# Optimization experiments

Measured on AMD Instinct MI355X. Metric: run time of the kernel, lower is better.

Reference implementation:

```python
import jax, jax.numpy as jnp
import numpy as np

NUM_HEADS = 8
QKV_DIM = 32
DIM = 256
MULTI_Q = QKV_DIM * NUM_HEADS  # 256
BN_EPS = 1e-5


def conv1x1_bn(x, W, gamma, beta, mean, var):
    # 1x1 conv (no bias) followed by BatchNorm2d in eval mode.
    y = jnp.einsum('bchw,oc->bohw', x, W)
    inv = gamma / jnp.sqrt(var + BN_EPS)
    return y * inv[None, :, None, None] + (beta - mean * inv)[None, :, None, None]


def setup_inputs() -> dict:
    key = jax.random.key(0)
    ks = jax.random.split(key, 16)
    B, C, H, W = 16, DIM, 64, 64
    inp = {
        'input_': jax.random.normal(ks[0], (B, C, H, W), jnp.float32),
        'key_v_input_reduction': jax.random.normal(ks[1], (B, C, 32, 32), jnp.float32),
        # to_q: Conv2d_BN(dim -> multi_q_dim)
        'Wq': jax.random.normal(ks[2], (MULTI_Q, DIM), jnp.float32) * 0.05,
        'gq': jnp.ones((MULTI_Q,), jnp.float32),
        'bq': jnp.zeros((MULTI_Q,), jnp.float32),
        'mq': jax.random.normal(ks[3], (MULTI_Q,), jnp.float32) * 0.1,
        'vq': jax.random.uniform(ks[4], (MULTI_Q,), jnp.float32, 0.5, 1.5),
        # to_kv: Conv2d_BN(dim -> qkv_dim) (one_kv_head=True, share_kv=True)
        'Wkv': jax.random.normal(ks[5], (QKV_DIM, DIM), jnp.float32) * 0.05,
        'gkv': jnp.ones((QKV_DIM,), jnp.float32),
        'bkv': jnp.zeros((QKV_DIM,), jnp.float32),
        'mkv': jax.random.normal(ks[6], (QKV_DIM,), jnp.float32) * 0.1,
        'vkv': jax.random.uniform(ks[7], (QKV_DIM,), jnp.float32, 0.5, 1.5),
        # proj: activation -> Conv2d_BN(multi_q_dim -> dim)
        'Wp': jax.random.normal(ks[8], (DIM, MULTI_Q), jnp.float32) * 0.05,
        'gp': jnp.ones((DIM,), jnp.float32),
        'bp': jnp.zeros((DIM,), jnp.float32),
        'mp': jax.random.normal(ks[9], (DIM,), jnp.float32) * 0.1,
        'vp': jax.random.uniform(ks[10], (DIM,), jnp.float32, 0.5, 1.5),
    }
    return inp


def reference(input_, key_v_input_reduction, Wq, gq, bq, mq, vq,
              Wkv, gkv, bkv, mkv, vkv, Wp, gp, bp, mp, vp):
    B, C, H, W = input_.shape
    HW = H * W
    # Q projection -> (B, nh, d, HW)
    queries = conv1x1_bn(input_, Wq, gq, bq, mq, vq).reshape(B, NUM_HEADS, QKV_DIM, HW)
    # shared K=V projection, single kv head -> (B, 1, d, HW)
    kv = conv1x1_bn(input_, Wkv, gkv, bkv, mkv, vkv).reshape(B, 1, QKV_DIM, HW)
    key = jax.nn.softmax(kv, axis=3)       # softmax over spatial positions
    query = jax.nn.softmax(queries, axis=2)  # softmax over channel dim
    value = kv
    # context = key @ value^T : (B,1,d,d)
    context = jnp.einsum('bhdn,bhen->bhde', key, value)
    # permute(0,1,3,2) then broadcast over heads, attended = context^T @ query
    ctx_t = jnp.swapaxes(context, -1, -2)   # (B,1,d,d)
    attended = jnp.einsum('bhde,bken->bkdn'.replace('h', 'o'), ctx_t[:, 0][:, None], query) if False else jnp.matmul(ctx_t, query)  # (B,nh,d,HW) via broadcast
    attended = attended.reshape(B, MULTI_Q, H, W)
    # proj: ReLU then Conv2d_BN
    out = conv1x1_bn(jax.nn.relu(attended), Wp, gp, bp, mp, vp)
    return out
```

## Files before the change

### kernel.cpp

```cpp
#include <hip/hip_runtime.h>
#include <hip/hip_bf16.h>
#include <cstdint>

typedef _Float16 f16;
typedef _Float16 f16x4 __attribute__((ext_vector_type(4)));
typedef _Float16 f16x8 __attribute__((ext_vector_type(8)));
typedef float f32x4 __attribute__((ext_vector_type(4)));

#define MFMA16(a, b, c) __builtin_amdgcn_mfma_f32_16x16x32_f16((a), (b), (c), 0, 0, 0)

constexpr int BATCH = 16;
constexpr int C     = 256;
constexpr int HW    = 4096;
constexpr int DH    = 32;
constexpr int MR    = 288;
constexpr float EPS = 1e-5f;

constexpr size_t OFF_XT = 0;
constexpr size_t SZ_XT  = (size_t)BATCH * HW * C * 2;
constexpr size_t OFF_KV = OFF_XT + SZ_XT;
constexpr size_t SZ_KV  = (size_t)BATCH * DH * HW * 4;
constexpr size_t OFF_W1 = OFF_KV + SZ_KV;
constexpr size_t SZ_W1  = (size_t)MR * C * 2;
constexpr size_t OFF_B1 = OFF_W1 + SZ_W1;
constexpr size_t OFF_WP = OFF_B1 + 2048;
constexpr size_t SZ_WP  = (size_t)C * C * 2;
constexpr size_t OFF_BP = OFF_WP + SZ_WP;
constexpr size_t OFF_RM = OFF_BP + 1024;
constexpr size_t OFF_RS = OFF_RM + 2048;
constexpr size_t OFF_U  = OFF_RS + 2048;

__global__ __launch_bounds__(256) void k0_prep(
    const float* __restrict__ Wq,  const float* __restrict__ gq,  const float* __restrict__ bq,
    const float* __restrict__ mq,  const float* __restrict__ vq,
    const float* __restrict__ Wkv, const float* __restrict__ gkv, const float* __restrict__ bkv,
    const float* __restrict__ mkv, const float* __restrict__ vkv,
    const float* __restrict__ Wp,  const float* __restrict__ gp,  const float* __restrict__ bp,
    const float* __restrict__ mp,  const float* __restrict__ vp,
    f16* __restrict__ W1, float* __restrict__ b1, f16* __restrict__ Wp2, float* __restrict__ bp2) {
  int id = blockIdx.x * 256 + threadIdx.x;
  if (id < 65536) {
    int o = id >> 8, c = id & 255;
    float inv = gq[o] * rsqrtf(vq[o] + EPS);
    W1[o * 256 + c] = (f16)(Wq[o * 256 + c] * inv);
  } else if (id < 73728) {
    int o = (id - 65536) >> 8, c = id & 255;
    float inv = gkv[o] * rsqrtf(vkv[o] + EPS);
    W1[(256 + o) * 256 + c] = (f16)(Wkv[o * 256 + c] * inv);
  } else if (id < 139264) {
    int o = (id - 73728) >> 8, c = id & 255;
    float inv = gp[o] * rsqrtf(vp[o] + EPS);
    Wp2[o * 256 + c] = (f16)(Wp[o * 256 + c] * inv);
  } else if (id < 139552) {
    int r = id - 139264;
    if (r < 256) { float inv = gq[r] * rsqrtf(vq[r] + EPS);   b1[r] = bq[r] - mq[r] * inv; }
    else { int e = r - 256; float inv = gkv[e] * rsqrtf(vkv[e] + EPS); b1[r] = bkv[e] - mkv[e] * inv; }
  } else if (id < 139808) {
    int o = id - 139552;
    float inv = gp[o] * rsqrtf(vp[o] + EPS);
    bp2[o] = bp[o] - mp[o] * inv;
  }
}

__global__ __launch_bounds__(256, 3) void p0_trans_kv(
    const float* __restrict__ X, const f16* __restrict__ Wkv2, const float* __restrict__ bkv1,
    f16* __restrict__ XT, float* __restrict__ kvo) {
  __shared__ alignas(16) f16 xt[64 * 264];
  __shared__ alignas(16) float kvb[32 * 68];
  const int t = threadIdx.x, b = blockIdx.y, n0 = blockIdx.x * 64;
  const int lane = t & 63, w = t >> 6, l15 = lane & 15, quad = lane >> 4;
  const float* Xb = X + (size_t)b * C * HW;

  {
    int c4 = (t & 15) * 4, n4 = (t >> 4) * 4;
#pragma unroll
    for (int ci = 0; ci < 4; ++ci) {
      int c0 = ci * 64 + c4;
      const float* xp = Xb + (size_t)c0 * HW + n0 + n4;
      float4 v0 = *(const float4*)&xp[0];
      float4 v1 = *(const float4*)&xp[HW];
      float4 v2 = *(const float4*)&xp[2 * HW];
      float4 v3 = *(const float4*)&xp[3 * HW];
      f16x4 w0 = {(f16)v0.x, (f16)v1.x, (f16)v2.x, (f16)v3.x};
      f16x4 w1 = {(f16)v0.y, (f16)v1.y, (f16)v2.y, (f16)v3.y};
      f16x4 w2 = {(f16)v0.z, (f16)v1.z, (f16)v2.z, (f16)v3.z};
      f16x4 w3 = {(f16)v0.w, (f16)v1.w, (f16)v2.w, (f16)v3.w};
      *(f16x4*)&xt[(n4 + 0) * 264 + c0] = w0;
      *(f16x4*)&xt[(n4 + 1) * 264 + c0] = w1;
      *(f16x4*)&xt[(n4 + 2) * 264 + c0] = w2;
      *(f16x4*)&xt[(n4 + 3) * 264 + c0] = w3;
    }
  }
  __syncthreads();

#pragma unroll
  for (int i = 0; i < 8; ++i) {
    int u = t + i * 256, row = u >> 5, seg = u & 31;
    f16x8 v = *(const f16x8*)&xt[row * 264 + seg * 8];
    *(f16x8*)&XT[((size_t)b * HW + n0 + row) * 256 + seg * 8] = v;
  }

  f32x4 acc0, acc1;
  {
    float bv0 = bkv1[l15], bv1 = bkv1[16 + l15];
#pragma unroll
    for (int r = 0; r < 4; ++r) { acc0[r] = bv0; acc1[r] = bv1; }
  }
#pragma unroll
  for (int kc = 0; kc < 8; ++kc) {
    f16x8 af  = *(const f16x8*)&xt[(w * 16 + l15) * 264 + kc * 32 + quad * 8];
    f16x8 bf0 = *(const f16x8*)&Wkv2[l15 * 256 + kc * 32 + quad * 8];
    f16x8 bf1 = *(const f16x8*)&Wkv2[(16 + l15) * 256 + kc * 32 + quad * 8];
    acc0 = MFMA16(af, bf0, acc0);
    acc1 = MFMA16(af, bf1, acc1);
  }
#pragma unroll
  for (int r = 0; r < 4; ++r) {
    int n = w * 16 + quad * 4 + r;
    kvb[l15 * 68 + n] = acc0[r];
    kvb[(16 + l15) * 68 + n] = acc1[r];
  }
  __syncthreads();
#pragma unroll
  for (int i = 0; i < 2; ++i) {
    int u = t + i * 256, d = u >> 4, seg = u & 15;
    float4 v = *(const float4*)&kvb[d * 68 + seg * 4];
    *(float4*)&kvo[((size_t)b * DH + d) * HW + n0 + seg * 4] = v;
  }
}

__global__ __launch_bounds__(256) void k2_stats(
    const float* __restrict__ kv, float* __restrict__ rowmax, float* __restrict__ rowsum) {
  int r = blockIdx.x, t = threadIdx.x, w = t >> 6, lane = t & 63;
  const float4* row = (const float4*)(kv + (size_t)r * HW);
  float4 v0 = row[t], v1 = row[t + 256], v2 = row[t + 512], v3 = row[t + 768];
  float m = fmaxf(fmaxf(fmaxf(v0.x, v0.y), fmaxf(v0.z, v0.w)),
                  fmaxf(fmaxf(v1.x, v1.y), fmaxf(v1.z, v1.w)));
  m = fmaxf(m, fmaxf(fmaxf(fmaxf(v2.x, v2.y), fmaxf(v2.z, v2.w)),
                     fmaxf(fmaxf(v3.x, v3.y), fmaxf(v3.z, v3.w))));
  for (int off = 32; off; off >>= 1) m = fmaxf(m, __shfl_xor(m, off));
  __shared__ float sm[4], ss[4];
  if (lane == 0) sm[w] = m;
  __syncthreads();
  m = fmaxf(fmaxf(sm[0], sm[1]), fmaxf(sm[2], sm[3]));
  float s = __expf(v0.x - m) + __expf(v0.y - m) + __expf(v0.z - m) + __expf(v0.w - m)
          + __expf(v1.x - m) + __expf(v1.y - m) + __expf(v1.z - m) + __expf(v1.w - m)
          + __expf(v2.x - m) + __expf(v2.y - m) + __expf(v2.z - m) + __expf(v2.w - m)
          + __expf(v3.x - m) + __expf(v3.y - m) + __expf(v3.z - m) + __expf(v3.w - m);
  for (int off = 32; off; off >>= 1) s += __shfl_xor(s, off);
  if (lane == 0) ss[w] = s;
  __syncthreads();
  if (t == 0) { rowmax[r] = m; rowsum[r] = ss[0] + ss[1] + ss[2] + ss[3]; }
}

__global__ __launch_bounds__(256, 4) void k3_ctx(
    const float* __restrict__ kv, const float* __restrict__ rowmax,
    const float* __restrict__ rowsum, float* __restrict__ U) {
  __shared__ float cacc[32 * 33];
  const int t = threadIdx.x, b = blockIdx.y;
  const int lane = t & 63, w = t >> 6, l15 = lane & 15, quad = lane >> 4;
  for (int i = t; i < 32 * 33; i += 256) cacc[i] = 0.f;
  __syncthreads();
  const float* kvb = kv + (size_t)b * DH * HW;
  float M0 = rowmax[b * 32 + l15],      Si0 = 1.f / rowsum[b * 32 + l15];
  float M1 = rowmax[b * 32 + 16 + l15], Si1 = 1.f / rowsum[b * 32 + 16 + l15];
  f32x4 acc[2][2] = {};
#pragma unroll
  for (int s = 0; s < 4; ++s) {
    int nb = blockIdx.x * 512 + w * 128 + s * 32 + quad * 8;
    const float* p0 = &kvb[(size_t)l15 * HW + nb];
    const float* p1 = &kvb[(size_t)(16 + l15) * HW + nb];
    float lo[8], hi[8];
    *(float4*)&lo[0] = *(const float4*)&p0[0]; *(float4*)&lo[4] = *(const float4*)&p0[4];
    *(float4*)&hi[0] = *(const float4*)&p1[0]; *(float4*)&hi[4] = *(const float4*)&p1[4];
    f16x8 A0, A1, B0, B1;
#pragma unroll
    for (int j = 0; j < 8; ++j) {
      A0[j] = (f16)lo[j]; A1[j] = (f16)hi[j];
      B0[j] = (f16)(__expf(lo[j] - M0) * Si0);
      B1[j] = (f16)(__expf(hi[j] - M1) * Si1);
    }
    acc[0][0] = MFMA16(A0, B0, acc[0][0]);
    acc[1][0] = MFMA16(A1, B0, acc[1][0]);
    acc[0][1] = MFMA16(A0, B1, acc[0][1]);
    acc[1][1] = MFMA16(A1, B1, acc[1][1]);
  }
#pragma unroll
  for (int a = 0; a < 2; ++a)
#pragma unroll
    for (int e2 = 0; e2 < 2; ++e2)
#pragma unroll
      for (int r = 0; r < 4; ++r)
        atomicAdd(&cacc[(a * 16 + quad * 4 + r) * 33 + e2 * 16 + l15], acc[a][e2][r]);
  __syncthreads();
  for (int i = t; i < 1024; i += 256)
    atomicAdd(&U[b * 1024 + (i >> 5) * 32 + (i & 31)], cacc[(i >> 5) * 33 + (i & 31)]);
}

__global__ __launch_bounds__(256, 2) void kb_mega(
    const f16* __restrict__ XT, const f16* __restrict__ Wq2, const float* __restrict__ bq1,
    const float* __restrict__ U, const f16* __restrict__ Wp2, const float* __restrict__ bp1,
    float* __restrict__ out) {
  __shared__ alignas(16) f16 xs[64 * 40];
  __shared__ alignas(16) f16 wsv[256 * 40];
  __shared__ alignas(16) f16 pa[64 * 264];
  __shared__ alignas(16) f16 ctxs[32 * 40];
  const int t = threadIdx.x, b = blockIdx.y, n0 = blockIdx.x * 64;
  const int lane = t & 63, w = t >> 6, l15 = lane & 15, quad = lane >> 4;
  const int wn = w & 1, wm = w >> 1;

  {
    const float4 u4 = *(const float4*)&U[b * 1024 + t * 4];
    int d = t >> 3, e4 = (t & 7) * 4;
    f16x4 pk = {(f16)u4.x, (f16)u4.y, (f16)u4.z, (f16)u4.w};
    *(f16x4*)&ctxs[d * 40 + e4] = pk;
  }
  const f16* XTb = XT + ((size_t)b * HW + n0) * 256;
  const int sr = t >> 2, ss = t & 3;

  f32x4 acc1[2][8];
#pragma unroll
  for (int nf = 0; nf < 8; ++nf) {
    float bv = bq1[wn * 128 + nf * 16 + l15];
#pragma unroll
    for (int mf = 0; mf < 2; ++mf)
#pragma unroll
      for (int r = 0; r < 4; ++r) acc1[mf][nf][r] = bv;
  }
#pragma unroll 1
  for (int kc = 0; kc < 8; ++kc) {
    f16x8 vx, vw[4];
    vx = *(const f16x8*)&XTb[(size_t)sr * 256 + kc * 32 + ss * 8];
#pragma unroll
    for (int i = 0; i < 4; ++i)
      vw[i] = *(const f16x8*)&Wq2[(size_t)(sr + i * 64) * 256 + kc * 32 + ss * 8];
    __syncthreads();
    *(f16x8*)&xs[sr * 40 + ss * 8] = vx;
#pragma unroll
    for (int i = 0; i < 4; ++i) *(f16x8*)&wsv[(sr + i * 64) * 40 + ss * 8] = vw[i];
    __syncthreads();
    f16x8 a0 = *(const f16x8*)&xs[(wm * 32 + l15) * 40 + quad * 8];
    f16x8 a1 = *(const f16x8*)&xs[(wm * 32 + 16 + l15) * 40 + quad * 8];
#pragma unroll
    for (int nf = 0; nf < 8; ++nf) {
      f16x8 bf = *(const f16x8*)&wsv[(wn * 128 + nf * 16 + l15) * 40 + quad * 8];
      acc1[0][nf] = MFMA16(a0, bf, acc1[0][nf]);
      acc1[1][nf] = MFMA16(a1, bf, acc1[1][nf]);
    }
  }

#pragma unroll
  for (int mf = 0; mf < 2; ++mf)
#pragma unroll
    for (int h = 0; h < 4; ++h) {
      f32x4 v0 = acc1[mf][h * 2], v1 = acc1[mf][h * 2 + 1];
      f32x4 mx;
#pragma unroll
      for (int r = 0; r < 4; ++r) mx[r] = fmaxf(v0[r], v1[r]);
#pragma unroll
      for (int off = 1; off <= 8; off <<= 1)
#pragma unroll
        for (int r = 0; r < 4; ++r) mx[r] = fmaxf(mx[r], __shfl_xor(mx[r], off));
      f32x4 s4;
#pragma unroll
      for (int r = 0; r < 4; ++r) {
        v0[r] = __expf(v0[r] - mx[r]); v1[r] = __expf(v1[r] - mx[r]);
        s4[r] = v0[r] + v1[r];
      }
#pragma unroll
      for (int off = 1; off <= 8; off <<= 1)
#pragma unroll
        for (int r = 0; r < 4; ++r) s4[r] += __shfl_xor(s4[r], off);
      int o0 = wn * 128 + h * 32 + l15;
#pragma unroll
      for (int r = 0; r < 4; ++r) {
        int n = wm * 32 + mf * 16 + quad * 4 + r;
        float si = 1.f / s4[r];
        pa[n * 264 + o0]      = (f16)(v0[r] * si);
        pa[n * 264 + o0 + 16] = (f16)(v1[r] * si);
      }
    }
  __syncthreads();

  f32x4 datt[2][2][4] = {};
#pragma unroll
  for (int hh = 0; hh < 2; ++hh) {
    int h = w * 2 + hh;
#pragma unroll
    for (int mt = 0; mt < 2; ++mt) {
      f16x8 af = *(const f16x8*)&ctxs[(mt * 16 + l15) * 40 + quad * 8];
#pragma unroll
      for (int nt = 0; nt < 4; ++nt) {
        f16x8 bf = *(const f16x8*)&pa[(nt * 16 + l15) * 264 + h * 32 + quad * 8];
        datt[hh][mt][nt] = MFMA16(af, bf, datt[hh][mt][nt]);
      }
    }
  }
#pragma unroll
  for (int hh = 0; hh < 2; ++hh) {
    int h = w * 2 + hh;
#pragma unroll
    for (int mt = 0; mt < 2; ++mt)
#pragma unroll
      for (int nt = 0; nt < 4; ++nt)
#pragma unroll
        for (int r = 0; r < 4; ++r) {
          int n = nt * 16 + l15;
          int cc = h * 32 + mt * 16 + quad * 4 + r;
          pa[n * 264 + cc] = (f16)fmaxf(datt[hh][mt][nt][r], 0.f);
        }
  }
  __syncthreads();

  f32x4 acc2[8][2];
#pragma unroll
  for (int mf = 0; mf < 8; ++mf)
#pragma unroll
    for (int r = 0; r < 4; ++r) {
      float bv = bp1[wm * 128 + mf * 16 + quad * 4 + r];
      acc2[mf][0][r] = bv; acc2[mf][1][r] = bv;
    }
#pragma unroll 1
  for (int kc = 0; kc < 8; ++kc) {
    f16x8 vw[4];
#pragma unroll
    for (int i = 0; i < 4; ++i)
      vw[i] = *(const f16x8*)&Wp2[(size_t)(sr + i * 64) * 256 + kc * 32 + ss * 8];
    __syncthreads();
#pragma unroll
    for (int i = 0; i < 4; ++i) *(f16x8*)&wsv[(sr + i * 64) * 40 + ss * 8] = vw[i];
    __syncthreads();
    f16x8 bf0 = *(const f16x8*)&pa[(wn * 32 + l15) * 264 + kc * 32 + quad * 8];
    f16x8 bf1 = *(const f16x8*)&pa[(wn * 32 + 16 + l15) * 264 + kc * 32 + quad * 8];
#pragma unroll
    for (int mf = 0; mf < 8; ++mf) {
      f16x8 af = *(const f16x8*)&wsv[(wm * 128 + mf * 16 + l15) * 40 + quad * 8];
      acc2[mf][0] = MFMA16(af, bf0, acc2[mf][0]);
      acc2[mf][1] = MFMA16(af, bf1, acc2[mf][1]);
    }
  }
#pragma unroll
  for (int mf = 0; mf < 8; ++mf)
#pragma unroll
    for (int nf = 0; nf < 2; ++nf) {
      int n = n0 + wn * 32 + nf * 16 + l15;
#pragma unroll
      for (int r = 0; r < 4; ++r) {
        int o = wm * 128 + mf * 16 + quad * 4 + r;
        out[((size_t)b * C + o) * HW + n] = acc2[mf][nf][r];
      }
    }
}

extern "C" void kernel_launch(void* const* d_in, const int* in_sizes, int n_in,
                              void* d_out, int out_size, void* d_ws, size_t ws_size,
                              hipStream_t stream) {
  (void)in_sizes; (void)n_in; (void)out_size; (void)ws_size;
  const float* input = (const float*)d_in[0];
  const float* Wq  = (const float*)d_in[2];
  const float* gq  = (const float*)d_in[3];
  const float* bq  = (const float*)d_in[4];
  const float* mq  = (const float*)d_in[5];
  const float* vq  = (const float*)d_in[6];
  const float* Wkv = (const float*)d_in[7];
  const float* gkv = (const float*)d_in[8];
  const float* bkv = (const float*)d_in[9];
  const float* mkv = (const float*)d_in[10];
  const float* vkv = (const float*)d_in[11];
  const float* Wp  = (const float*)d_in[12];
  const float* gp  = (const float*)d_in[13];
  const float* bp  = (const float*)d_in[14];
  const float* mp  = (const float*)d_in[15];
  const float* vp  = (const float*)d_in[16];

  char* ws = (char*)d_ws;
  f16*   XTw = (f16*)(ws + OFF_XT);
  float* kvw = (float*)(ws + OFF_KV);
  f16*   W1  = (f16*)(ws + OFF_W1);
  float* b1  = (float*)(ws + OFF_B1);
  f16*   Wp2 = (f16*)(ws + OFF_WP);
  float* bp2 = (float*)(ws + OFF_BP);
  float* rm  = (float*)(ws + OFF_RM);
  float* rs  = (float*)(ws + OFF_RS);
  float* U   = (float*)(ws + OFF_U);
  float* out = (float*)d_out;

  const f16* Wq2  = W1;
  const f16* Wkv2 = W1 + 65536;
  const float* bq1  = b1;
  const float* bkv1 = b1 + 256;

  hipMemsetAsync(U, 0, (size_t)BATCH * DH * DH * 4, stream);
  k0_prep<<<547, 256, 0, stream>>>(Wq, gq, bq, mq, vq, Wkv, gkv, bkv, mkv, vkv,
                                   Wp, gp, bp, mp, vp, W1, b1, Wp2, bp2);
  p0_trans_kv<<<dim3(64, 16), 256, 0, stream>>>(input, Wkv2, bkv1, XTw, kvw);
  k2_stats<<<512, 256, 0, stream>>>(kvw, rm, rs);
  k3_ctx<<<dim3(8, 16), 256, 0, stream>>>(kvw, rm, rs, U);
  kb_mega<<<dim3(64, 16), 256, 0, stream>>>(XTw, Wq2, bq1, U, Wp2, bp2, out);
}
```

Measured before the change: 224.4 us.

## Drop LDS weight staging in kb_mega, alias LDS in p0, widen k3 grid

kb_mega stops staging Wq/Wp tiles through shared memory with per-chunk double barriers. It now loads the whole 64x256 X tile into the pa buffer once and reads the weight fragments straight from global memory (L2-resident), with launch bounds raised to 4 blocks per CU. p0_trans_kv reuses the xt LDS buffer for kvb behind an added barrier so more blocks fit per CU, and k3_ctx uses twice as many blocks, each doing half the work. The aim is fewer barriers and less LDS per block for higher occupancy, at the cost of redundant uncoalesced global weight loads and possible register pressure under the tighter bounds.

Result: slower. 248.0 us (+10.5%).

```diff
diff --git a/kernel.cpp b/kernel.cpp
--- a/kernel.cpp
+++ b/kernel.cpp
@@ -62,11 +62,11 @@
   }
 }
 
-__global__ __launch_bounds__(256, 3) void p0_trans_kv(
+__global__ __launch_bounds__(256, 4) void p0_trans_kv(
     const float* __restrict__ X, const f16* __restrict__ Wkv2, const float* __restrict__ bkv1,
     f16* __restrict__ XT, float* __restrict__ kvo) {
   __shared__ alignas(16) f16 xt[64 * 264];
-  __shared__ alignas(16) float kvb[32 * 68];
+  float* kvb = (float*)xt;
   const int t = threadIdx.x, b = blockIdx.y, n0 = blockIdx.x * 64;
   const int lane = t & 63, w = t >> 6, l15 = lane & 15, quad = lane >> 4;
   const float* Xb = X + (size_t)b * C * HW;
@@ -114,6 +114,7 @@
     acc0 = MFMA16(af, bf0, acc0);
     acc1 = MFMA16(af, bf1, acc1);
   }
+  __syncthreads();
 #pragma unroll
   for (int r = 0; r < 4; ++r) {
     int n = w * 16 + quad * 4 + r;
@@ -166,8 +167,8 @@
   float M1 = rowmax[b * 32 + 16 + l15], Si1 = 1.f / rowsum[b * 32 + 16 + l15];
   f32x4 acc[2][2] = {};
 #pragma unroll
-  for (int s = 0; s < 4; ++s) {
-    int nb = blockIdx.x * 512 + w * 128 + s * 32 + quad * 8;
+  for (int s = 0; s < 2; ++s) {
+    int nb = blockIdx.x * 256 + w * 64 + s * 32 + quad * 8;
     const float* p0 = &kvb[(size_t)l15 * HW + nb];
     const float* p1 = &kvb[(size_t)(16 + l15) * HW + nb];
     float lo[8], hi[8];
@@ -197,26 +198,28 @@
     atomicAdd(&U[b * 1024 + (i >> 5) * 32 + (i & 31)], cacc[(i >> 5) * 33 + (i & 31)]);
 }
 
-__global__ __launch_bounds__(256, 2) void kb_mega(
+__global__ __launch_bounds__(256, 4) void kb_mega(
     const f16* __restrict__ XT, const f16* __restrict__ Wq2, const float* __restrict__ bq1,
     const float* __restrict__ U, const f16* __restrict__ Wp2, const float* __restrict__ bp1,
     float* __restrict__ out) {
-  __shared__ alignas(16) f16 xs[64 * 40];
-  __shared__ alignas(16) f16 wsv[256 * 40];
   __shared__ alignas(16) f16 pa[64 * 264];
   __shared__ alignas(16) f16 ctxs[32 * 40];
   const int t = threadIdx.x, b = blockIdx.y, n0 = blockIdx.x * 64;
   const int lane = t & 63, w = t >> 6, l15 = lane & 15, quad = lane >> 4;
   const int wn = w & 1, wm = w >> 1;
-
+  const f16* XTb = XT + ((size_t)b * HW + n0) * 256;
+
+#pragma unroll
+  for (int i = 0; i < 8; ++i) {
+    int u = t + i * 256, row = u >> 5, seg = u & 31;
+    *(f16x8*)&pa[row * 264 + seg * 8] = *(const f16x8*)&XTb[(size_t)row * 256 + seg * 8];
+  }
   {
     const float4 u4 = *(const float4*)&U[b * 1024 + t * 4];
     int d = t >> 3, e4 = (t & 7) * 4;
     f16x4 pk = {(f16)u4.x, (f16)u4.y, (f16)u4.z, (f16)u4.w};
     *(f16x4*)&ctxs[d * 40 + e4] = pk;
   }
-  const f16* XTb = XT + ((size_t)b * HW + n0) * 256;
-  const int sr = t >> 2, ss = t & 3;
 
   f32x4 acc1[2][8];
 #pragma unroll
@@ -227,27 +230,19 @@
 #pragma unroll
       for (int r = 0; r < 4; ++r) acc1[mf][nf][r] = bv;
   }
-#pragma unroll 1
+  __syncthreads();
+#pragma unroll 2
   for (int kc = 0; kc < 8; ++kc) {
-    f16x8 vx, vw[4];
-    vx = *(const f16x8*)&XTb[(size_t)sr * 256 + kc * 32 + ss * 8];
-#pragma unroll
-    for (int i = 0; i < 4; ++i)
-      vw[i] = *(const f16x8*)&Wq2[(size_t)(sr + i * 64) * 256 + kc * 32 + ss * 8];
-    __syncthreads();
-    *(f16x8*)&xs[sr * 40 + ss * 8] = vx;
-#pragma unroll
-    for (int i = 0; i < 4; ++i) *(f16x8*)&wsv[(sr + i * 64) * 40 + ss * 8] = vw[i];
-    __syncthreads();
-    f16x8 a0 = *(const f16x8*)&xs[(wm * 32 + l15) * 40 + quad * 8];
-    f16x8 a1 = *(const f16x8*)&xs[(wm * 32 + 16 + l15) * 40 + quad * 8];
+    f16x8 a0 = *(const f16x8*)&pa[(wm * 32 + l15) * 264 + kc * 32 + quad * 8];
+    f16x8 a1 = *(const f16x8*)&pa[(wm * 32 + 16 + l15) * 264 + kc * 32 + quad * 8];
 #pragma unroll
     for (int nf = 0; nf < 8; ++nf) {
-      f16x8 bf = *(const f16x8*)&wsv[(wn * 128 + nf * 16 + l15) * 40 + quad * 8];
+      f16x8 bf = *(const f16x8*)&Wq2[(size_t)(wn * 128 + nf * 16 + l15) * 256 + kc * 32 + quad * 8];
       acc1[0][nf] = MFMA16(a0, bf, acc1[0][nf]);
       acc1[1][nf] = MFMA16(a1, bf, acc1[1][nf]);
     }
   }
+  __syncthreads();
 
 #pragma unroll
   for (int mf = 0; mf < 2; ++mf)
@@ -320,21 +315,13 @@
       float bv = bp1[wm * 128 + mf * 16 + quad * 4 + r];
       acc2[mf][0][r] = bv; acc2[mf][1][r] = bv;
     }
-#pragma unroll 1
+#pragma unroll 2
   for (int kc = 0; kc < 8; ++kc) {
-    f16x8 vw[4];
-#pragma unroll
-    for (int i = 0; i < 4; ++i)
-      vw[i] = *(const f16x8*)&Wp2[(size_t)(sr + i * 64) * 256 + kc * 32 + ss * 8];
-    __syncthreads();
-#pragma unroll
-    for (int i = 0; i < 4; ++i) *(f16x8*)&wsv[(sr + i * 64) * 40 + ss * 8] = vw[i];
-    __syncthreads();
     f16x8 bf0 = *(const f16x8*)&pa[(wn * 32 + l15) * 264 + kc * 32 + quad * 8];
     f16x8 bf1 = *(const f16x8*)&pa[(wn * 32 + 16 + l15) * 264 + kc * 32 + quad * 8];
 #pragma unroll
     for (int mf = 0; mf < 8; ++mf) {
-      f16x8 af = *(const f16x8*)&wsv[(wm * 128 + mf * 16 + l15) * 40 + quad * 8];
+      f16x8 af = *(const f16x8*)&Wp2[(size_t)(wm * 128 + mf * 16 + l15) * 256 + kc * 32 + quad * 8];
       acc2[mf][0] = MFMA16(af, bf0, acc2[mf][0]);
       acc2[mf][1] = MFMA16(af, bf1, acc2[mf][1]);
     }
@@ -395,6 +382,6 @@
                                    Wp, gp, bp, mp, vp, W1, b1, Wp2, bp2);
   p0_trans_kv<<<dim3(64, 16), 256, 0, stream>>>(input, Wkv2, bkv1, XTw, kvw);
   k2_stats<<<512, 256, 0, stream>>>(kvw, rm, rs);
-  k3_ctx<<<dim3(8, 16), 256, 0, stream>>>(kvw, rm, rs, U);
+  k3_ctx<<<dim3(16, 16), 256, 0, stream>>>(kvw, rm, rs, U);
   kb_mega<<<dim3(64, 16), 256, 0, stream>>>(XTw, Wq2, bq1, U, Wp2, bp2, out);
 }
```
